# Performance work log

Hardware: AMD Instinct MI355X
Metric: run time of the kernel (lower is better)

The kernel has to match this reference:

```python
import math
import jax, jax.numpy as jnp
import numpy as np

B, T, E = 2, 2048, 4096
H, HKV = 32, 8
DH = E // H          # 128
G = H // HKV         # 4

ROPE_THETA = 500000.0
ROPE_FACTOR = 32.0
HI_FREQ_FACTOR = 4.0
LO_FREQ_FACTOR = 1.0
ORIG_CTX = 8192


def setup_inputs() -> dict:
    key = jax.random.key(0)
    kx, kq, kk, kv, ko = jax.random.split(key, 5)
    w = lambda k, shape: jax.random.normal(k, shape, jnp.float32) * 0.02
    return {
        "x": jax.random.normal(kx, (B, T, E), jnp.float32),
        # torch nn.Linear stores weight as [out, in]; y = x @ W.T
        "Wq": w(kq, (E, E)),
        "Wk": w(kk, (HKV * DH, E)),
        "Wv": w(kv, (HKV * DH, E)),
        "Wo": w(ko, (E, E)),
    }


def _rope_cos_sin(t_len):
    # faithful port of Llama3MHAttention._rope_cos_sin (llama3 rope scaling)
    inv_freq = 1.0 / (ROPE_THETA ** (jnp.arange(0, DH, 2, dtype=jnp.float32) / DH))
    wavelen = 2.0 * math.pi / inv_freq
    cut_lo = ORIG_CTX / HI_FREQ_FACTOR   # wavelen_cutoff[0]
    cut_hi = ORIG_CTX / LO_FREQ_FACTOR   # wavelen_cutoff[1]
    inv_freq = jnp.where(wavelen > cut_hi, inv_freq / ROPE_FACTOR, inv_freq)
    smooth = (ORIG_CTX / wavelen - LO_FREQ_FACTOR) / (HI_FREQ_FACTOR - LO_FREQ_FACTOR)
    smoothed = (1.0 - smooth) * inv_freq / ROPE_FACTOR + smooth * inv_freq
    # exactly as in the source: ~(wavelen < cutoff[1]) & ~(wavelen > cutoff[0])
    is_medium = (~(wavelen < cut_hi)) & (~(wavelen > cut_lo))
    inv_freq = jnp.where(is_medium, smoothed, inv_freq)
    pos = jnp.arange(t_len, dtype=jnp.float32)          # T_past = 0
    freqs = pos[:, None] * inv_freq[None, :]            # [T, DH/2]
    emb = jnp.concatenate([freqs, freqs], axis=-1)      # [T, DH]
    return jnp.cos(emb), jnp.sin(emb)


def _rotate_half(x):
    x1, x2 = jnp.split(x, 2, axis=-1)
    return jnp.concatenate([-x2, x1], axis=-1)


def reference(x, Wq, Wk, Wv, Wo):
    b, t, _ = x.shape
    q = (x @ Wq.T).reshape(b, t, H, DH).transpose(0, 2, 1, 3)      # [B,H,T,Dh]
    k = (x @ Wk.T).reshape(b, t, HKV, DH).transpose(0, 2, 1, 3)    # [B,Hkv,T,Dh]
    v = (x @ Wv.T).reshape(b, t, HKV, DH).transpose(0, 2, 1, 3)    # [B,Hkv,T,Dh]

    cos, sin = _rope_cos_sin(t)
    cos = cos.astype(x.dtype)[None, None]   # [1,1,T,Dh]
    sin = sin.astype(x.dtype)[None, None]
    q = q * cos + _rotate_half(q) * sin
    k = k * cos + _rotate_half(k) * sin

    qg = q.reshape(b, HKV, G, t, DH)                                # GQA grouping
    scores = jnp.einsum(
        'bhgtd,bhkd->bhgtk', qg.astype(jnp.float32), k.astype(jnp.float32)
    ) / math.sqrt(DH)                                               # [B,Hkv,G,T,T] fp32
    causal = jnp.tril(jnp.ones((t, t), dtype=bool))
    scores = jnp.where(causal[None, None, None], scores,
                       jnp.finfo(jnp.float32).min)
    attn = jax.nn.softmax(scores, axis=-1).astype(x.dtype)
    ctx = jnp.einsum('bhgtk,bhkd->bhgtd', attn, v)                  # [B,Hkv,G,T,Dh]
    out = ctx.reshape(b, H, t, DH).transpose(0, 2, 1, 3).reshape(b, t, E)
    return out @ Wo.T
```

## Files before the change

### kernel.cpp

```cpp
#include <hip/hip_runtime.h>
#include <cstdint>
#include <cstddef>


typedef __bf16 bf16_t;
typedef float  f32x4  __attribute__((ext_vector_type(4)));
typedef __bf16 bf16x8 __attribute__((ext_vector_type(8)));
typedef __bf16 bf16x4 __attribute__((ext_vector_type(4)));

static constexpr int kB   = 2;
static constexpr int kT   = 2048;
static constexpr int kE   = 4096;
static constexpr int kH   = 32;
static constexpr int kHKV = 8;
static constexpr int kDH  = 128;
static constexpr int kNQKV = kE + 2 * kHKV * kDH;
static constexpr int kM    = kB * kT;

__device__ __forceinline__ void gll16(const void* g, void* l) {
  __builtin_amdgcn_global_load_lds(
      (__attribute__((address_space(1))) void*)g,
      (__attribute__((address_space(3))) void*)l, 16, 0, 0);
}

__global__ void cast_f32_bf16_k(const float* __restrict__ in,
                                bf16_t* __restrict__ out, int n4) {
  int i = blockIdx.x * 256 + threadIdx.x;
  if (i >= n4) return;
  float4 v = reinterpret_cast<const float4*>(in)[i];
  bf16x4 o;
  o[0] = (__bf16)v.x; o[1] = (__bf16)v.y; o[2] = (__bf16)v.z; o[3] = (__bf16)v.w;
  reinterpret_cast<bf16x4*>(out)[i] = o;
}

__global__ void rope_table_k(float* __restrict__ cosT, float* __restrict__ sinT) {
  int idx = blockIdx.x * 256 + threadIdx.x;
  if (idx >= kT * 64) return;
  int t = idx >> 6, i = idx & 63;
  float ex  = (float)i / 64.0f;
  float inv = powf(500000.0f, -ex);
  float wl  = 6.283185307179586f / inv;
  const float cut_lo = 8192.0f / 4.0f;
  const float cut_hi = 8192.0f / 1.0f;
  float inv2 = (wl > cut_hi) ? inv * (1.0f / 32.0f) : inv;
  float smooth   = (8192.0f / wl - 1.0f) * (1.0f / 3.0f);
  float smoothed = (1.0f - smooth) * inv2 * (1.0f / 32.0f) + smooth * inv2;
  bool  medium   = (!(wl < cut_hi)) && (!(wl > cut_lo));
  float invf = medium ? smoothed : inv2;
  float f = (float)t * invf;
  cosT[idx] = cosf(f);
  sinT[idx] = sinf(f);
}

__global__ void rope_q_k(const bf16_t* __restrict__ QKV,
                         const float* __restrict__ cosT,
                         const float* __restrict__ sinT,
                         bf16_t* __restrict__ Qr) {
  int idx = blockIdx.x * 256 + threadIdx.x;
  if (idx >= kB * kT * kH * 64) return;
  int i = idx & 63;
  int h = (idx >> 6) & 31;
  int t = (idx >> 11) & 2047;
  int b = idx >> 22;
  const bf16_t* src = QKV + (size_t)(b * kT + t) * kNQKV + h * kDH + i;
  float q1 = (float)src[0], q2 = (float)src[64];
  float c = cosT[(t << 6) + i], s = sinT[(t << 6) + i];
  const float sc = 0.08838834764831845f;
  bf16_t* dst = Qr + ((size_t)(b * kH + h) * kT + t) * kDH + i;
  dst[0]  = (__bf16)((q1 * c - q2 * s) * sc);
  dst[64] = (__bf16)((q2 * c + q1 * s) * sc);
}

__global__ void rope_k_k(const bf16_t* __restrict__ QKV,
                         const float* __restrict__ cosT,
                         const float* __restrict__ sinT,
                         bf16_t* __restrict__ Kr) {
  int idx = blockIdx.x * 256 + threadIdx.x;
  if (idx >= kB * kT * kHKV * 64) return;
  int i = idx & 63;
  int h = (idx >> 6) & 7;
  int t = (idx >> 9) & 2047;
  int b = idx >> 20;
  const bf16_t* src = QKV + (size_t)(b * kT + t) * kNQKV + kE + h * kDH + i;
  float k1 = (float)src[0], k2 = (float)src[64];
  float c = cosT[(t << 6) + i], s = sinT[(t << 6) + i];
  bf16_t* dst = Kr + ((size_t)(b * kHKV + h) * kT + t) * kDH + i;
  dst[0]  = (__bf16)(k1 * c - k2 * s);
  dst[64] = (__bf16)(k2 * c + k1 * s);
}

__global__ void vtrans_k(const bf16_t* __restrict__ QKV, bf16_t* __restrict__ Vt) {
  __shared__ bf16_t tile[64 * 130];
  int bidx = blockIdx.x;
  int tt = bidx & 31;
  int h  = (bidx >> 5) & 7;
  int b  = bidx >> 8;
  int tid = threadIdx.x;
  int t0 = tt * 64;
  for (int it = 0; it < 32; ++it) {
    int e = it * 256 + tid;
    int tr = e >> 7, d = e & 127;
    tile[tr * 130 + d] =
        QKV[(size_t)(b * kT + t0 + tr) * kNQKV + kE + kHKV * kDH + h * kDH + d];
  }
  __syncthreads();
  for (int j = 0; j < 32; ++j) {
    int o = j * 256 + tid;
    int d = o >> 6, tr = o & 63;
    Vt[((size_t)(b * kHKV + h) * kDH + d) * kT + t0 + tr] = tile[tr * 130 + d];
  }
}

template <bool OUT_BF16>
__global__ __launch_bounds__(256, 2)
void gemm_nt_k(const bf16_t* __restrict__ A, const bf16_t* __restrict__ Bm,
               void* __restrict__ Cv, int M, int N, int K) {
  __shared__ bf16_t As[128 * 32];
  __shared__ bf16_t Bs[128 * 32];
  const int tid = threadIdx.x;
  const int lane = tid & 63, wid = tid >> 6;
  const int l16 = lane & 15, lg = lane >> 4;
  const int row0 = blockIdx.x * 128, col0 = blockIdx.y * 128;
  const int wr = wid >> 1, wc = wid & 1;

  const int s_row = wid * 16 + (lane >> 2);
  const int s_col = (lane & 3) * 8;
  const bf16_t* Ag = A  + (size_t)(row0 + s_row) * K + s_col;
  const bf16_t* Bg = Bm + (size_t)(col0 + s_row) * K + s_col;
  char* AsB = (char*)As + wid * 1024;
  char* BsB = (char*)Bs + wid * 1024;

  const int aoff0 = (wr * 64 + l16) * 32 + lg * 8;
  const int boff0 = (wc * 64 + l16) * 32 + lg * 8;

  f32x4 acc[4][4] = {};
  for (int kt = 0; kt < K; kt += 32) {
    gll16(Ag + kt,                 AsB);
    gll16(Ag + kt + (size_t)64 * K, AsB + 4096);
    gll16(Bg + kt,                 BsB);
    gll16(Bg + kt + (size_t)64 * K, BsB + 4096);
    __syncthreads();
    bf16x8 af[4], bfr[4];
#pragma unroll
    for (int m = 0; m < 4; ++m)
      af[m] = *reinterpret_cast<const bf16x8*>(&As[aoff0 + m * 512]);
#pragma unroll
    for (int n = 0; n < 4; ++n)
      bfr[n] = *reinterpret_cast<const bf16x8*>(&Bs[boff0 + n * 512]);
#pragma unroll
    for (int m = 0; m < 4; ++m)
#pragma unroll
      for (int n = 0; n < 4; ++n)
        acc[m][n] = __builtin_amdgcn_mfma_f32_16x16x32_bf16(af[m], bfr[n],
                                                            acc[m][n], 0, 0, 0);
    __syncthreads();
  }

  const int crow = row0 + wr * 64 + lg * 4;
  const int ccol = col0 + wc * 64 + l16;
#pragma unroll
  for (int m = 0; m < 4; ++m)
#pragma unroll
    for (int n = 0; n < 4; ++n)
#pragma unroll
      for (int j = 0; j < 4; ++j) {
        size_t idx = (size_t)(crow + m * 16 + j) * N + (ccol + n * 16);
        if constexpr (OUT_BF16)
          ((bf16_t*)Cv)[idx] = (__bf16)acc[m][n][j];
        else
          ((float*)Cv)[idx] = acc[m][n][j];
      }
}

__global__ __launch_bounds__(256, 2)
void flash_k(const bf16_t* __restrict__ Qr, const bf16_t* __restrict__ Kr,
             const bf16_t* __restrict__ Vt, bf16_t* __restrict__ Ctx) {
  __shared__ bf16_t Ks[2][64 * 128];
  __shared__ bf16_t Vs[2][128 * 64];
  __shared__ bf16_t Ps[4][32 * 64];

  const int gid  = blockIdx.x;
  const int wgid = (gid & 7) * 128 + (gid >> 3);
  const int qt = 15 - (wgid & 15);
  const int h  = (wgid >> 4) & 31;
  const int b  = wgid >> 9;
  const int hkv = h >> 2;
  const int tid = threadIdx.x, lane = tid & 63, w = tid >> 6;
  const int l16 = lane & 15, lg = lane >> 4;
  const int qbase = qt * 128;

  const bf16_t* Qg = Qr +
      ((size_t)(b * kH + h) * kT + qbase + w * 32 + l16) * kDH + lg * 8;
  bf16x8 qf[2][4];
#pragma unroll
  for (int m = 0; m < 2; ++m)
#pragma unroll
    for (int kk = 0; kk < 4; ++kk)
      qf[m][kk] = *reinterpret_cast<const bf16x8*>(Qg + m * 16 * kDH + kk * 32);

  const bf16_t* Kg = Kr + (size_t)(b * kHKV + hkv) * kT * kDH;
  const bf16_t* Vg = Vt + (size_t)(b * kHKV + hkv) * kDH * kT;

  const int k_srow = w * 4 + lg;
  const int k_scolb = l16 * 16;
  const int v_srow = w * 8 + (lane >> 3);
  const int v_scolb = (lane & 7) * 16;

  float m_run[2][4], l_run[2][4];
#pragma unroll
  for (int m = 0; m < 2; ++m)
#pragma unroll
    for (int j = 0; j < 4; ++j) { m_run[m][j] = -1e30f; l_run[m][j] = 0.f; }
  f32x4 acc_o[2][8] = {};

  const int nkv = 2 * qt + 2;

#pragma unroll
  for (int r = 0; r < 4; ++r) {
    int krow = r * 16 + k_srow;
    int kcb  = k_scolb ^ ((krow & 7) << 4);
    gll16(Kg + (size_t)krow * kDH + (kcb >> 1),
          (char*)Ks[0] + w * 1024 + r * 4096);
    int vrow = r * 32 + v_srow;
    int vcb  = v_scolb ^ ((vrow & 7) << 4);
    gll16(Vg + (size_t)vrow * kT + (vcb >> 1),
          (char*)Vs[0] + w * 1024 + r * 4096);
  }

  for (int it = 0; it < nkv; ++it) {
    const int cur = it & 1;
    const int kv0 = it * 64;
    asm volatile("s_waitcnt vmcnt(0)" ::: "memory");
    __builtin_amdgcn_s_barrier();
    __builtin_amdgcn_sched_barrier(0);
    if (it + 1 < nkv) {
      const int kv1 = kv0 + 64;
#pragma unroll
      for (int r = 0; r < 4; ++r) {
        int krow = r * 16 + k_srow;
        int kcb  = k_scolb ^ ((krow & 7) << 4);
        gll16(Kg + (size_t)(kv1 + krow) * kDH + (kcb >> 1),
              (char*)Ks[cur ^ 1] + w * 1024 + r * 4096);
        int vrow = r * 32 + v_srow;
        int vcb  = v_scolb ^ ((vrow & 7) << 4);
        gll16(Vg + (size_t)vrow * kT + kv1 + (vcb >> 1),
              (char*)Vs[cur ^ 1] + w * 1024 + r * 4096);
      }
    }

    f32x4 sc[2][4] = {};
#pragma unroll
    for (int kk = 0; kk < 4; ++kk) {
#pragma unroll
      for (int nf = 0; nf < 4; ++nf) {
        int row = nf * 16 + l16;
        int cb  = (kk * 64 + lg * 16) ^ ((row & 7) << 4);
        bf16x8 kf = *reinterpret_cast<const bf16x8*>(
            (const char*)Ks[cur] + row * 256 + cb);
#pragma unroll
        for (int m = 0; m < 2; ++m)
          sc[m][nf] = __builtin_amdgcn_mfma_f32_16x16x32_bf16(
              qf[m][kk], kf, sc[m][nf], 0, 0, 0);
      }
    }
    if (it >= nkv - 2) {
#pragma unroll
      for (int nf = 0; nf < 4; ++nf) {
        int key = kv0 + nf * 16 + l16;
#pragma unroll
        for (int m = 0; m < 2; ++m)
#pragma unroll
          for (int j = 0; j < 4; ++j) {
            int qrow = qbase + w * 32 + m * 16 + lg * 4 + j;
            if (key > qrow) sc[m][nf][j] = -1e30f;
          }
      }
    }
#pragma unroll
    for (int m = 0; m < 2; ++m)
#pragma unroll
      for (int j = 0; j < 4; ++j) {
        float mx = fmaxf(fmaxf(sc[m][0][j], sc[m][1][j]),
                         fmaxf(sc[m][2][j], sc[m][3][j]));
        mx = fmaxf(mx, __shfl_xor(mx, 1));
        mx = fmaxf(mx, __shfl_xor(mx, 2));
        mx = fmaxf(mx, __shfl_xor(mx, 4));
        mx = fmaxf(mx, __shfl_xor(mx, 8));
        float mnew = fmaxf(m_run[m][j], mx);
        float alpha = __expf(m_run[m][j] - mnew);
        m_run[m][j] = mnew;
        float ssum = 0.f;
#pragma unroll
        for (int nf = 0; nf < 4; ++nf) {
          float p = __expf(sc[m][nf][j] - mnew);
          sc[m][nf][j] = p;
          ssum += p;
        }
        ssum += __shfl_xor(ssum, 1);
        ssum += __shfl_xor(ssum, 2);
        ssum += __shfl_xor(ssum, 4);
        ssum += __shfl_xor(ssum, 8);
        l_run[m][j] = l_run[m][j] * alpha + ssum;
#pragma unroll
        for (int nf = 0; nf < 8; ++nf) acc_o[m][nf][j] *= alpha;
      }
#pragma unroll
    for (int m = 0; m < 2; ++m)
#pragma unroll
      for (int j = 0; j < 4; ++j) {
        int prow = m * 16 + lg * 4 + j;
        int swz  = (prow & 7) << 4;
#pragma unroll
        for (int nf = 0; nf < 4; ++nf) {
          int wbyte = ((nf * 16 + l16) * 2) ^ swz;
          *(bf16_t*)((char*)Ps[w] + prow * 128 + wbyte) = (__bf16)sc[m][nf][j];
        }
      }
#pragma unroll
    for (int kk2 = 0; kk2 < 2; ++kk2) {
      bf16x8 pf[2];
#pragma unroll
      for (int m = 0; m < 2; ++m) {
        int prow = m * 16 + l16;
        int cb = (kk2 * 64 + lg * 16) ^ ((prow & 7) << 4);
        pf[m] = *reinterpret_cast<const bf16x8*>(
            (const char*)Ps[w] + prow * 128 + cb);
      }
#pragma unroll
      for (int nf = 0; nf < 8; ++nf) {
        int d = nf * 16 + l16;
        int cb = (kk2 * 64 + lg * 16) ^ ((d & 7) << 4);
        bf16x8 vf = *reinterpret_cast<const bf16x8*>(
            (const char*)Vs[cur] + d * 128 + cb);
#pragma unroll
        for (int m = 0; m < 2; ++m)
          acc_o[m][nf] = __builtin_amdgcn_mfma_f32_16x16x32_bf16(
              pf[m], vf, acc_o[m][nf], 0, 0, 0);
      }
    }
  }

#pragma unroll
  for (int m = 0; m < 2; ++m) {
    const int tglob = qbase + w * 32 + m * 16 + lg * 4;
#pragma unroll
    for (int j = 0; j < 4; ++j) {
      float inv_l = 1.0f / l_run[m][j];
#pragma unroll
      for (int nf = 0; nf < 8; ++nf)
        Ctx[((size_t)(b * kT + tglob + j) * kH + h) * kDH + nf * 16 + l16] =
            (__bf16)(acc_o[m][nf][j] * inv_l);
    }
  }
}

extern "C" void kernel_launch(void* const* d_in, const int* in_sizes, int n_in,
                              void* d_out, int out_size, void* d_ws, size_t ws_size,
                              hipStream_t stream) {
  (void)in_sizes; (void)n_in; (void)out_size; (void)ws_size;
  const float* x  = (const float*)d_in[0];
  const float* Wq = (const float*)d_in[1];
  const float* Wk = (const float*)d_in[2];
  const float* Wv = (const float*)d_in[3];
  const float* Wo = (const float*)d_in[4];
  float* out = (float*)d_out;

  char* ws = (char*)d_ws;
  size_t off = 0;
  auto alloc = [&](size_t bytes) -> char* {
    char* p = ws + off;
    off += (bytes + 255) & ~(size_t)255;
    return p;
  };
  bf16_t* xb    = (bf16_t*)alloc((size_t)kM * kE * 2);
  bf16_t* Wqkvb = (bf16_t*)alloc((size_t)kNQKV * kE * 2);
  bf16_t* Wob   = (bf16_t*)alloc((size_t)kE * kE * 2);
  bf16_t* QKV   = (bf16_t*)alloc((size_t)kM * kNQKV * 2);
  float*  cosT  = (float*)alloc((size_t)kT * 64 * 4);
  float*  sinT  = (float*)alloc((size_t)kT * 64 * 4);
  bf16_t* Qr  = Wqkvb;
  bf16_t* Kr  = Wqkvb + (size_t)kE * kE;
  bf16_t* Vt  = Wqkvb + (size_t)(kE + kHKV * kDH) * kE;
  bf16_t* Ctx = xb;

  cast_f32_bf16_k<<<16384, 256, 0, stream>>>(x, xb, kM * kE / 4);
  cast_f32_bf16_k<<<16384, 256, 0, stream>>>(Wq, Wqkvb, kE * kE / 4);
  cast_f32_bf16_k<<<4096, 256, 0, stream>>>(Wk, Wqkvb + (size_t)kE * kE,
                                            kHKV * kDH * kE / 4);
  cast_f32_bf16_k<<<4096, 256, 0, stream>>>(Wv, Wqkvb + (size_t)(kE + kHKV * kDH) * kE,
                                            kHKV * kDH * kE / 4);
  cast_f32_bf16_k<<<16384, 256, 0, stream>>>(Wo, Wob, kE * kE / 4);
  rope_table_k<<<512, 256, 0, stream>>>(cosT, sinT);

  {
    dim3 g(kM / 128, kNQKV / 128);
    gemm_nt_k<true><<<g, 256, 0, stream>>>(xb, Wqkvb, QKV, kM, kNQKV, kE);
  }
  rope_q_k<<<32768, 256, 0, stream>>>(QKV, cosT, sinT, Qr);
  rope_k_k<<<8192, 256, 0, stream>>>(QKV, cosT, sinT, Kr);
  vtrans_k<<<512, 256, 0, stream>>>(QKV, Vt);
  flash_k<<<kB * kH * (kT / 128), 256, 0, stream>>>(Qr, Kr, Vt, Ctx);
  {
    dim3 g(kM / 128, kE / 128);
    gemm_nt_k<false><<<g, 256, 0, stream>>>(Ctx, Wob, out, kM, kE, kE);
  }
}
```

Baseline: 854.8 us.

## Restructure GEMM into 256x256 tiles with 4-stage async LDS pipeline

```diff
diff --git a/kernel.cpp b/kernel.cpp
--- a/kernel.cpp
+++ b/kernel.cpp
@@ -112,54 +112,93 @@
 }
 
 template <bool OUT_BF16>
-__global__ __launch_bounds__(256, 2)
+__global__ __launch_bounds__(512, 2)
 void gemm_nt_k(const bf16_t* __restrict__ A, const bf16_t* __restrict__ Bm,
                void* __restrict__ Cv, int M, int N, int K) {
-  __shared__ bf16_t As[128 * 32];
-  __shared__ bf16_t Bs[128 * 32];
+  extern __shared__ char smem[];
   const int tid = threadIdx.x;
   const int lane = tid & 63, wid = tid >> 6;
   const int l16 = lane & 15, lg = lane >> 4;
-  const int row0 = blockIdx.x * 128, col0 = blockIdx.y * 128;
-  const int wr = wid >> 1, wc = wid & 1;
-
-  const int s_row = wid * 16 + (lane >> 2);
-  const int s_col = (lane & 3) * 8;
-  const bf16_t* Ag = A  + (size_t)(row0 + s_row) * K + s_col;
-  const bf16_t* Bg = Bm + (size_t)(col0 + s_row) * K + s_col;
-  char* AsB = (char*)As + wid * 1024;
-  char* BsB = (char*)Bs + wid * 1024;
-
-  const int aoff0 = (wr * 64 + l16) * 32 + lg * 8;
-  const int boff0 = (wc * 64 + l16) * 32 + lg * 8;
-
-  f32x4 acc[4][4] = {};
-  for (int kt = 0; kt < K; kt += 32) {
-    gll16(Ag + kt,                 AsB);
-    gll16(Ag + kt + (size_t)64 * K, AsB + 4096);
-    gll16(Bg + kt,                 BsB);
-    gll16(Bg + kt + (size_t)64 * K, BsB + 4096);
-    __syncthreads();
-    bf16x8 af[4], bfr[4];
-#pragma unroll
-    for (int m = 0; m < 4; ++m)
-      af[m] = *reinterpret_cast<const bf16x8*>(&As[aoff0 + m * 512]);
+  const int wm = wid >> 2, wn = wid & 3;
+
+  const int nwg = gridDim.x;
+  const int bid = blockIdx.x;
+  const int wg = (bid & 7) * (nwg >> 3) + (bid >> 3);
+  const int colT = wg >> 4, rowT = wg & 15;
+  const int row0 = rowT * 256, col0 = colT * 256;
+
+  const int P0 = (wid << 10) + (lane << 4);
+  const int P1 = P0 + 8192;
+  const int r0 = P0 >> 6, kb0 = (P0 & 63) ^ (((P0 >> 7) & 3) << 4);
+  const int r1 = P1 >> 6, kb1 = (P1 & 63) ^ (((P1 >> 7) & 3) << 4);
+  const bf16_t* Ag0 = A  + (size_t)(row0 + r0) * K + (kb0 >> 1);
+  const bf16_t* Ag1 = A  + (size_t)(row0 + r1) * K + (kb1 >> 1);
+  const bf16_t* Bg0 = Bm + (size_t)(col0 + r0) * K + (kb0 >> 1);
+  const bf16_t* Bg1 = Bm + (size_t)(col0 + r1) * K + (kb1 >> 1);
+
+  char* const AsBase = smem;
+  char* const BsBase = smem + 65536;
+  const int woff = wid << 10;
+
+  auto stage = [&](int t, int b) {
+    const int kt = t << 5;
+    char* As = AsBase + (b << 14);
+    char* Bs = BsBase + (b << 14);
+    gll16(Ag0 + kt, As + woff);
+    gll16(Ag1 + kt, As + 8192 + woff);
+    gll16(Bg0 + kt, Bs + woff);
+    gll16(Bg1 + kt, Bs + 8192 + woff);
+  };
+
+  int aoffB[8], boffB[4];
+#pragma unroll
+  for (int m = 0; m < 8; ++m) {
+    int r = wm * 128 + m * 16 + l16;
+    aoffB[m] = r * 64 + ((lg ^ ((r >> 1) & 3)) << 4);
+  }
+#pragma unroll
+  for (int n = 0; n < 4; ++n) {
+    int r = wn * 64 + n * 16 + l16;
+    boffB[n] = r * 64 + ((lg ^ ((r >> 1) & 3)) << 4);
+  }
+
+  f32x4 acc[8][4] = {};
+  const int NT = K >> 5;
+
+  stage(0, 0); stage(1, 1); stage(2, 2);
+
+  for (int t = 0; t < NT; ++t) {
+    asm volatile("s_waitcnt vmcnt(8)\n\ts_barrier" ::: "memory");
+    __builtin_amdgcn_sched_barrier(0);
+    const int tp = t + 3;
+    stage(tp < NT ? tp : NT - 1, tp & 3);
+    __builtin_amdgcn_sched_barrier(0);
+
+    const char* As = AsBase + ((t & 3) << 14);
+    const char* Bs = BsBase + ((t & 3) << 14);
+    bf16x8 af[8], bf[4];
+#pragma unroll
+    for (int m = 0; m < 8; ++m)
+      af[m] = *reinterpret_cast<const bf16x8*>(As + aoffB[m]);
 #pragma unroll
     for (int n = 0; n < 4; ++n)
-      bfr[n] = *reinterpret_cast<const bf16x8*>(&Bs[boff0 + n * 512]);
-#pragma unroll
-    for (int m = 0; m < 4; ++m)
+      bf[n] = *reinterpret_cast<const bf16x8*>(Bs + boffB[n]);
+    __builtin_amdgcn_s_setprio(1);
+#pragma unroll
+    for (int m = 0; m < 8; ++m)
 #pragma unroll
       for (int n = 0; n < 4; ++n)
-        acc[m][n] = __builtin_amdgcn_mfma_f32_16x16x32_bf16(af[m], bfr[n],
+        acc[m][n] = __builtin_amdgcn_mfma_f32_16x16x32_bf16(af[m], bf[n],
                                                             acc[m][n], 0, 0, 0);
-    __syncthreads();
-  }
-
-  const int crow = row0 + wr * 64 + lg * 4;
-  const int ccol = col0 + wc * 64 + l16;
-#pragma unroll
-  for (int m = 0; m < 4; ++m)
+    __builtin_amdgcn_s_setprio(0);
+    __builtin_amdgcn_sched_barrier(0);
+  }
+  asm volatile("s_waitcnt vmcnt(0)" ::: "memory");
+
+  const int crow = row0 + wm * 128 + lg * 4;
+  const int ccol = col0 + wn * 64 + l16;
+#pragma unroll
+  for (int m = 0; m < 8; ++m)
 #pragma unroll
     for (int n = 0; n < 4; ++n)
 #pragma unroll
@@ -364,6 +403,11 @@
   const float* Wv = (const float*)d_in[3];
   const float* Wo = (const float*)d_in[4];
   float* out = (float*)d_out;
+
+  hipFuncSetAttribute((const void*)gemm_nt_k<true>,
+                      hipFuncAttributeMaxDynamicSharedMemorySize, 131072);
+  hipFuncSetAttribute((const void*)gemm_nt_k<false>,
+                      hipFuncAttributeMaxDynamicSharedMemorySize, 131072);
 
   char* ws = (char*)d_ws;
   size_t off = 0;
@@ -392,16 +436,12 @@
   cast_f32_bf16_k<<<16384, 256, 0, stream>>>(Wo, Wob, kE * kE / 4);
   rope_table_k<<<512, 256, 0, stream>>>(cosT, sinT);
 
-  {
-    dim3 g(kM / 128, kNQKV / 128);
-    gemm_nt_k<true><<<g, 256, 0, stream>>>(xb, Wqkvb, QKV, kM, kNQKV, kE);
-  }
+  gemm_nt_k<true><<<(kM / 256) * (kNQKV / 256), 512, 131072, stream>>>(
+      xb, Wqkvb, QKV, kM, kNQKV, kE);
   rope_q_k<<<32768, 256, 0, stream>>>(QKV, cosT, sinT, Qr);
   rope_k_k<<<8192, 256, 0, stream>>>(QKV, cosT, sinT, Kr);
   vtrans_k<<<512, 256, 0, stream>>>(QKV, Vt);
   flash_k<<<kB * kH * (kT / 128), 256, 0, stream>>>(Qr, Kr, Vt, Ctx);
-  {
-    dim3 g(kM / 128, kE / 128);
-    gemm_nt_k<false><<<g, 256, 0, stream>>>(Ctx, Wob, out, kM, kE, kE);
-  }
-}
+  gemm_nt_k<false><<<(kM / 256) * (kE / 256), 512, 131072, stream>>>(
+      Ctx, Wob, out, kM, kE, kE);
+}
```

After: 813.4 us. 1.05x faster.
